# Optimization experiments

Measured on AMD Instinct MI355X. Metric: run time of the kernel, lower is better.

The kernel has to match this reference:

```python
import jax, jax.numpy as jnp
import numpy as np

B_, N, C, H = 512, 49, 256, 8
DH = C // H            # 32
RB, NRF = 8, 32
NWIN = B_ // RB        # 64
DC = 64                # class_token_dim
TC = C + 2 * DC        # 384
WS = 7
SCALE = DH ** -0.5


def _rel_pos_index():
    ch = np.arange(WS)
    coords = np.stack(np.meshgrid(ch, ch, indexing='ij')).reshape(2, -1)  # [2,49]
    rel = (coords[:, :, None] - coords[:, None, :]).transpose(1, 2, 0)    # [49,49,2]
    rel[..., 0] += WS - 1
    rel[..., 1] += WS - 1
    rel[..., 0] *= 2 * WS - 1
    return jnp.asarray(rel.sum(-1).reshape(-1))  # [49*49]


def _ln(x, axes, eps=1e-5):
    m = x.mean(axes, keepdims=True)
    v = x.var(axes, keepdims=True)
    return (x - m) * jax.lax.rsqrt(v + eps)


def setup_inputs() -> dict:
    key = jax.random.key(0)
    ks = jax.random.split(key, 20)
    def w(i, shape, s=0.02):
        return jax.random.normal(ks[i], shape, jnp.float32) * s
    return dict(
        x=w(0, (B_, N, C), 1.0),
        x_ref=w(1, (RB, NRF, C), 1.0),
        depth_token=w(2, (B_, N, DC), 1.0),
        seg_token=w(3, (B_, N, DC), 1.0),
        qkv_w=w(4, (C, 3 * C)), qkv_b=jnp.zeros(3 * C, jnp.float32),
        proj_w=w(5, (C, C)), proj_b=jnp.zeros(C, jnp.float32),
        rel_bias=w(6, ((2 * WS - 1) ** 2, H)),
        diff_mu=w(7, (1, 1, C), 1.0), diff_logsigma=w(8, (1, 1, C)),
        ref_qk_w=w(9, (C, 2 * C)), ref_qk_b=jnp.zeros(2 * C, jnp.float32),
        conv_w=w(10, (H, H, 3, 3), 0.1), conv_b=jnp.zeros(H, jnp.float32),
        q_norm_w=jnp.ones(C, jnp.float32), q_norm_b=jnp.zeros(C, jnp.float32),
        q_proj_w=w(11, (C, C)), q_proj_b=jnp.zeros(C, jnp.float32),
        cls_dth_q_w=w(12, (DC, DC)), cls_dth_q_b=jnp.zeros(DC, jnp.float32),
        cls_seg_q_w=w(13, (DC, DC)), cls_seg_q_b=jnp.zeros(DC, jnp.float32),
        global_k_w=w(14, (TC, TC)), global_k_b=jnp.zeros(TC, jnp.float32),
        global_v_w=w(15, (TC, TC)), global_v_b=jnp.zeros(TC, jnp.float32),
        proj_dth_w=w(16, (DC, DC)), proj_dth_b=jnp.zeros(DC, jnp.float32),
    )


def reference(x, x_ref, depth_token, seg_token, qkv_w, qkv_b, proj_w, proj_b,
              rel_bias, diff_mu, diff_logsigma, ref_qk_w, ref_qk_b, conv_w, conv_b,
              q_norm_w, q_norm_b, q_proj_w, q_proj_b, cls_dth_q_w, cls_dth_q_b,
              cls_seg_q_w, cls_seg_q_b, global_k_w, global_k_b, global_v_w,
              global_v_b, proj_dth_w, proj_dth_b):
    # qkv: [B_,N,3C] -> q,k,v each [B_,H,N,DH]
    qkv = (x @ qkv_w + qkv_b).reshape(B_, N, 3, H, DH).transpose(2, 0, 3, 1, 4)
    q, k, v = qkv[0], qkv[1], qkv[2]

    # ---- group attention (ref branch) ----
    ref_qk = (x_ref @ ref_qk_w + ref_qk_b).reshape(RB, NRF, 2, C).transpose(2, 0, 1, 3)
    ref_q, ref_v = ref_qk[0], ref_qk[1]                       # [RB,NRF,C]
    ref_q = diff_mu + jnp.exp(diff_logsigma) * ref_q
    ref_q = ref_q.reshape(RB, NRF, H, DH).transpose(0, 2, 1, 3)  # [RB,H,NRF,DH]
    ref_v = ref_v.reshape(RB, NRF, H, DH).transpose(0, 2, 1, 3)

    qs = (q * SCALE).reshape(RB, NWIN, H, N, DH)
    # scores against shared (per-image) ref keys; avoids materializing repeated K
    ref_attn = jnp.einsum('rwhnd,rhfd->rhwnf', qs, ref_q)     # [RB,H,NWIN,N,NRF]
    ref_attn_r = ref_attn.reshape(RB, H, NWIN * N, NRF)
    # 3-step diffusion: conv2d over heads-as-channels + LN(no affine) + gelu, residual
    for _ in range(3):
        u = jax.lax.conv_general_dilated(
            ref_attn_r, conv_w, (1, 1), 'SAME',
            dimension_numbers=('NCHW', 'OIHW', 'NCHW')) + conv_b[None, :, None, None]
        u = jax.nn.gelu(_ln(u, (-2, -1)), approximate=False)
        ref_attn_r = ref_attn_r + u
    ref_attn = jax.nn.softmax(ref_attn_r.reshape(RB, H, NWIN, N, NRF), axis=-1)
    q_new = jnp.einsum('rhwnf,rhfd->rwnhd', ref_attn, ref_v).reshape(B_, N, C)
    q_sc = q.transpose(0, 2, 1, 3).reshape(B_, N, C)          # unscaled shortcut
    q_new = (_ln(q_new + q_sc, (-1,)) * q_norm_w + q_norm_b) @ q_proj_w + q_proj_b + q_sc
    q_new = q_new.reshape(B_, N, H, DH).transpose(0, 2, 1, 3) * SCALE

    # ---- window attention with relative position bias ----
    bias = rel_bias[_rel_pos_index()].reshape(N, N, H).transpose(2, 0, 1)  # [H,N,N]
    attn = jax.nn.softmax(jnp.einsum('bhnd,bhmd->bhnm', q_new, k) + bias[None], axis=-1)
    out = jnp.einsum('bhnm,bhmd->bnhd', attn, v).reshape(B_, N, C)
    out = out @ proj_w + proj_b

    # ---- class-token global attention ----
    dch = DC // H   # 8
    tdh = TC // H   # 48
    depth_q = (depth_token @ cls_dth_q_w + cls_dth_q_b).reshape(B_, N, H, dch).transpose(0, 2, 1, 3) * SCALE
    seg_q = (seg_token @ cls_seg_q_w + cls_seg_q_b).reshape(B_, N, H, dch).transpose(0, 2, 1, 3) * SCALE
    t_x = jnp.concatenate([out, depth_token, seg_token], axis=-1)  # [B_,N,TC]
    t_k = (t_x @ global_k_w + global_k_b).reshape(B_, N, H, tdh).transpose(0, 2, 1, 3)
    t_v = (t_x @ global_v_w + global_v_b).reshape(B_, N, H, tdh).transpose(0, 2, 1, 3)

    d_attn = jax.nn.softmax(jnp.einsum('bhnc,bhnt->bhct', depth_q, t_k), axis=-1)
    d_tok = jnp.einsum('bhct,bhnt->bhcn', d_attn, t_v).reshape(B_, DC, N).transpose(0, 2, 1)
    d_tok = d_tok @ proj_dth_w + proj_dth_b
    s_attn = jax.nn.softmax(jnp.einsum('bhnc,bhnt->bhct', seg_q, t_k), axis=-1)
    s_tok = jnp.einsum('bhct,bhnt->bhcn', s_attn, t_v).reshape(B_, DC, N).transpose(0, 2, 1)
    s_tok = s_tok @ proj_dth_w + proj_dth_b  # NOTE: original uses proj_dth for seg too
    return out, d_tok, s_tok
```

## Files before the change

### kernel.cpp

```cpp
#include <hip/hip_runtime.h>
#include <hip/hip_bf16.h>

typedef __hip_bfloat16 bf16;
typedef short s16x8 __attribute__((ext_vector_type(8)));
typedef float f32x4 __attribute__((ext_vector_type(4)));
union V16 { uint4 u4; s16x8 s8; unsigned u[4]; unsigned short s[8]; };

static __device__ __forceinline__ float b2f(bf16 v){ return __bfloat162float(v); }
static __device__ __forceinline__ bf16  f2b(float v){ return __float2bfloat16(v); }
static __device__ __forceinline__ unsigned short f2bs(float x){
    union { float f; unsigned u; } c; c.f = x;
    unsigned r = c.u + 0x7fff + ((c.u >> 16) & 1);
    return (unsigned short)(r >> 16);
}
static __device__ __forceinline__ float bu2f(unsigned short b){
    union { unsigned u; float f; } c; c.u = ((unsigned)b) << 16; return c.f;
}
static __device__ __forceinline__ s16x8 ld16g(const bf16* p){
    V16 u; u.u4 = *(const uint4*)p; return u.s8;
}
static __device__ __forceinline__ void glds16(const void* g, void* l){
    __builtin_amdgcn_global_load_lds(
        (const __attribute__((address_space(1))) unsigned*)g,
        (__attribute__((address_space(3))) unsigned*)l, 16, 0, 0);
}

#define SCALE_T 0.17677669529663687f

__global__ __launch_bounds__(256) void prep_weights(
    const float* __restrict__ qkvw, const float* __restrict__ qpw,
    const float* __restrict__ pw,   const float* __restrict__ gkw,
    const float* __restrict__ gvw,  bf16* __restrict__ Wt)
{
    int idx = blockIdx.x * 256 + threadIdx.x;
    float v;
    if (idx < 196608)      { int j = idx;          int n = j >> 8, k = j & 255; v = qkvw[k * 768 + n]; }
    else if (idx < 262144) { int j = idx - 196608; int n = j >> 8, k = j & 255; v = qpw[k * 256 + n]; }
    else if (idx < 327680) { int j = idx - 262144; int n = j >> 8, k = j & 255; v = pw[k * 256 + n]; }
    else if (idx < 475136) { int j = idx - 327680; int n = j / 384, k = j - n * 384; v = gkw[k * 384 + n]; }
    else                   { int j = idx - 475136; int n = j / 384, k = j - n * 384; v = gvw[k * 384 + n]; }
    ((unsigned short*)Wt)[idx] = f2bs(v);
}

__global__ __launch_bounds__(256) void convert_f32_bf16(
    const float* __restrict__ in, bf16* __restrict__ out)
{
    int i = blockIdx.x * 256 + threadIdx.x;
    float4 v = ((const float4*)in)[i];
    ushort4 o;
    o.x = f2bs(v.x); o.y = f2bs(v.y); o.z = f2bs(v.z); o.w = f2bs(v.w);
    ((ushort4*)out)[i] = o;
}

__global__ __launch_bounds__(256) void tok2b_kernel(
    const float* __restrict__ dth, const float* __restrict__ seg,
    bf16* __restrict__ tokb)
{
    int i = blockIdx.x * 256 + threadIdx.x;
    int row = i >> 4, j8 = i & 15;
    const float* src = (j8 < 8) ? (dth + (size_t)row * 64 + j8 * 8)
                                : (seg + (size_t)row * 64 + (j8 - 8) * 8);
    float4 u0 = ((const float4*)src)[0];
    float4 u1 = ((const float4*)src)[1];
    V16 o;
    o.s[0] = f2bs(u0.x); o.s[1] = f2bs(u0.y);
    o.s[2] = f2bs(u0.z); o.s[3] = f2bs(u0.w);
    o.s[4] = f2bs(u1.x); o.s[5] = f2bs(u1.y);
    o.s[6] = f2bs(u1.z); o.s[7] = f2bs(u1.w);
    *(uint4*)(tokb + (size_t)row * 128 + j8 * 8) = o.u4;
}

template<int TOK>
__global__ __launch_bounds__(256, 2) void gemm_pipe(
    const bf16* __restrict__ A, int lda, const bf16* __restrict__ A2,
    const bf16* __restrict__ Wt, const float* __restrict__ bias,
    const float* __restrict__ bias2,
    const bf16* __restrict__ addp, int addStride,
    float* __restrict__ outF, bf16* __restrict__ outB, int outStrideB,
    int K, int N, float scale)
{
    __shared__ char lds[4][16384];

    const int tid = threadIdx.x;
    const int wv = tid >> 6, lane = tid & 63;
    const int quad = lane >> 4, l15 = lane & 15;
    const int wr = wv >> 1, wc = wv & 1;

    const int gx = (int)gridDim.x;
    const int nwg = gx * (int)gridDim.y;
    int bid = (int)blockIdx.y * gx + (int)blockIdx.x;
    if ((nwg & 7) == 0) bid = (bid & 7) * (nwg >> 3) + (bid >> 3);
    const int bx = bid % gx, by = bid / gx;
    const int rowBase = by * 128, colBase = bx * 128;

    const int srow = tid >> 2;
    const int kOffE = (((tid & 3) ^ ((srow >> 1) & 3)) << 3);

    const unsigned swz = (unsigned)((quad ^ ((l15 >> 1) & 3)) << 4);
    const unsigned aoff0 = (unsigned)(wr * 4096 + l15 * 64) + swz;
    const unsigned boff0 = (unsigned)(wc * 4096 + l15 * 64) + swz;

    f32x4 acc[4][4];
    #pragma unroll
    for (int m = 0; m < 4; ++m)
        #pragma unroll
        for (int n = 0; n < 4; ++n)
            #pragma unroll
            for (int r = 0; r < 4; ++r) acc[m][n][r] = 0.f;

    const int nsteps = K >> 5;

    auto stageN = [&](int i) {
        int kt = i << 5;
        char* base = &lds[i & 3][0];
        #pragma unroll
        for (int c = 0; c < 2; ++c)
            glds16(Wt + (size_t)(colBase + c * 64 + srow) * K + (kt + kOffE),
                   base + 8192 + c * 4096 + tid * 16);
        if (!TOK || kt < 256) {
            #pragma unroll
            for (int c = 0; c < 2; ++c)
                glds16(A + (size_t)(rowBase + c * 64 + srow) * lda + (kt + kOffE),
                       base + c * 4096 + tid * 16);
        } else {
            #pragma unroll
            for (int c = 0; c < 2; ++c)
                glds16(A2 + (size_t)(rowBase + c * 64 + srow) * 128 + (kt - 256 + kOffE),
                       base + c * 4096 + tid * 16);
        }
    };

    stageN(0);
    if (nsteps > 1) stageN(1);
    if (nsteps > 2) stageN(2);

    for (int i = 0; i < nsteps; ++i) {
        int a = nsteps - 1 - i; if (a > 2) a = 2;
        if (a == 2)      asm volatile("s_waitcnt vmcnt(8)" ::: "memory");
        else if (a == 1) asm volatile("s_waitcnt vmcnt(4)" ::: "memory");
        else             asm volatile("s_waitcnt vmcnt(0)" ::: "memory");
        __builtin_amdgcn_sched_barrier(0);
        __builtin_amdgcn_s_barrier();
        __builtin_amdgcn_sched_barrier(0);

        if (i + 3 < nsteps) stageN(i + 3);

        const char* Ab2 = &lds[i & 3][0];
        const char* Bb2 = Ab2 + 8192;
        s16x8 af[4], bfr[4];
        #pragma unroll
        for (int m = 0; m < 4; ++m) af[m]  = *(const s16x8*)(Ab2 + aoff0 + m * 1024);
        #pragma unroll
        for (int n = 0; n < 4; ++n) bfr[n] = *(const s16x8*)(Bb2 + boff0 + n * 1024);
        #pragma unroll
        for (int m = 0; m < 4; ++m)
            #pragma unroll
            for (int n = 0; n < 4; ++n)
                acc[m][n] = __builtin_amdgcn_mfma_f32_16x16x32_bf16(af[m], bfr[n], acc[m][n], 0, 0, 0);
    }

    if (outB) {
        #pragma unroll
        for (int n = 0; n < 4; ++n) {
            int col = colBase + wc * 64 + n * 16 + l15;
            float bb = bias2 ? (col < 384 ? bias[col] : bias2[col - 384]) : bias[col];
            #pragma unroll
            for (int m = 0; m < 4; ++m) {
                #pragma unroll
                for (int r = 0; r < 4; ++r) {
                    int rl = wr * 64 + m * 16 + quad * 4 + r;
                    float v = acc[m][n][r] + bb;
                    if (addp) v += b2f(addp[(size_t)(rowBase + rl) * addStride + col]);
                    v *= scale;
                    if (outF) outF[(size_t)(rowBase + rl) * N + col] = v;
                    int cbyte = (wc * 64 + n * 16 + l15) * 2;
                    int blk = ((cbyte >> 5) ^ ((rl >> 2) & 7)) & 7;
                    *(unsigned short*)((char*)lds + rl * 256 + (blk << 5) + (cbyte & 31)) = f2bs(v);
                }
            }
        }
        __syncthreads();
        #pragma unroll
        for (int i = 0; i < 8; ++i) {
            int lin = i * 256 + tid;
            int rl = lin >> 4, cb = lin & 15;
            int cb2 = ((((cb >> 1) ^ ((rl >> 2) & 7)) & 7) << 1) | (cb & 1);
            uint4 val = *(const uint4*)((const char*)lds + rl * 256 + cb2 * 16);
            *(uint4*)(outB + (size_t)(rowBase + rl) * outStrideB + colBase + cb * 8) = val;
        }
    } else {
        #pragma unroll
        for (int n = 0; n < 4; ++n) {
            int col = colBase + wc * 64 + n * 16 + l15;
            float bb = bias2 ? (col < 384 ? bias[col] : bias2[col - 384]) : bias[col];
            #pragma unroll
            for (int m = 0; m < 4; ++m) {
                #pragma unroll
                for (int r = 0; r < 4; ++r) {
                    int rl = wr * 64 + m * 16 + quad * 4 + r;
                    float v = acc[m][n][r] + bb;
                    if (addp) v += b2f(addp[(size_t)(rowBase + rl) * addStride + col]);
                    v *= scale;
                    if (outF) outF[(size_t)(rowBase + rl) * N + col] = v;
                }
            }
        }
    }
}

template<int AF32, int OF32>
__global__ __launch_bounds__(256) void small64(
    const void* __restrict__ a0, const void* __restrict__ a1,
    const float* __restrict__ w0, const float* __restrict__ w1,
    const float* __restrict__ b0, const float* __restrict__ b1,
    void* __restrict__ o0, void* __restrict__ o1, float scale)
{
    __shared__ unsigned short WT[64 * 72];
    __shared__ float bsh[64];
    const int task = blockIdx.y;
    const void*  A    = task ? a1 : a0;
    const float* W    = task ? w1 : w0;
    const float* bias = task ? b1 : b0;
    void*        outp = task ? o1 : o0;

    int tid = threadIdx.x;
    for (int l = tid; l < 4096; l += 256) {
        int k = l >> 6, n = l & 63;
        WT[n * 72 + k] = f2bs(W[l]);
    }
    if (tid < 64) bsh[tid] = bias[tid];
    __syncthreads();

    const int wv = tid >> 6, lane = tid & 63;
    const int quad = lane >> 4, l15 = lane & 15;
    const int rowBase = blockIdx.x * 64;
    const int arow = rowBase + wv * 16 + l15;

    s16x8 a[2];
    if (AF32) {
        const float* Ar = (const float*)A + (size_t)arow * 64;
        #pragma unroll
        for (int ks = 0; ks < 2; ++ks) {
            float4 u0 = *(const float4*)(Ar + ks * 32 + quad * 8);
            float4 u1 = *(const float4*)(Ar + ks * 32 + quad * 8 + 4);
            V16 o;
            o.s[0] = f2bs(u0.x); o.s[1] = f2bs(u0.y);
            o.s[2] = f2bs(u0.z); o.s[3] = f2bs(u0.w);
            o.s[4] = f2bs(u1.x); o.s[5] = f2bs(u1.y);
            o.s[6] = f2bs(u1.z); o.s[7] = f2bs(u1.w);
            a[ks] = o.s8;
        }
    } else {
        const bf16* Ar = (const bf16*)A + (size_t)arow * 64;
        #pragma unroll
        for (int ks = 0; ks < 2; ++ks)
            a[ks] = ld16g(Ar + ks * 32 + quad * 8);
    }

    f32x4 acc[4];
    #pragma unroll
    for (int n = 0; n < 4; ++n)
        #pragma unroll
        for (int r = 0; r < 4; ++r) acc[n][r] = 0.f;

    #pragma unroll
    for (int ks = 0; ks < 2; ++ks)
        #pragma unroll
        for (int n = 0; n < 4; ++n) {
            s16x8 b = *(const s16x8*)&WT[(n * 16 + l15) * 72 + ks * 32 + quad * 8];
            acc[n] = __builtin_amdgcn_mfma_f32_16x16x32_bf16(a[ks], b, acc[n], 0, 0, 0);
        }

    #pragma unroll
    for (int n = 0; n < 4; ++n) {
        int col = n * 16 + l15;
        float bb = bsh[col];
        #pragma unroll
        for (int r = 0; r < 4; ++r) {
            int row = rowBase + wv * 16 + quad * 4 + r;
            float v = (acc[n][r] + bb) * scale;
            if (OF32) ((float*)outp)[(size_t)row * 64 + col] = v;
            else      ((bf16*)outp)[(size_t)row * 64 + col] = f2b(v);
        }
    }
}

__global__ __launch_bounds__(256) void mfma_gemm(
    const void* __restrict__ A, int a_mode,
    const float* __restrict__ W, const float* __restrict__ bias,
    float* __restrict__ outF, bf16* __restrict__ outB,
    int M, int K, int N, float scale)
{
    __shared__ __hip_bfloat16 Al[64][48];
    __shared__ __hip_bfloat16 Bl[64][48];

    const int tid  = threadIdx.x;
    const int wv   = tid >> 6, lane = tid & 63;
    const int quad = lane >> 4, l15 = lane & 15;
    const int rowBase = blockIdx.y * 64, colBase = blockIdx.x * 64;

    const int am = tid >> 2, ak = (tid & 3) * 8;
    const int bn = tid & 63, bk = (tid >> 6) * 8;

    f32x4 acc[4];
    #pragma unroll
    for (int t = 0; t < 4; ++t)
        #pragma unroll
        for (int r = 0; r < 4; ++r) acc[t][r] = 0.f;

    for (int kt = 0; kt < K; kt += 32) {
        s16x8 sa;
        if (a_mode == 1) {
            const bf16* Ab = (const bf16*)A;
            V16 u; u.u4 = *(const uint4*)(Ab + (size_t)(rowBase + am) * K + kt + ak);
            sa = u.s8;
        } else {
            const float* src = (const float*)A;
            const float4* p = (const float4*)(src + (size_t)(rowBase + am) * K + kt + ak);
            float4 u0 = p[0], u1 = p[1];
            sa[0] = (short)f2bs(u0.x); sa[1] = (short)f2bs(u0.y);
            sa[2] = (short)f2bs(u0.z); sa[3] = (short)f2bs(u0.w);
            sa[4] = (short)f2bs(u1.x); sa[5] = (short)f2bs(u1.y);
            sa[6] = (short)f2bs(u1.z); sa[7] = (short)f2bs(u1.w);
        }
        *(s16x8*)&Al[am][ak] = sa;

        s16x8 sb;
        #pragma unroll
        for (int j = 0; j < 8; ++j)
            sb[j] = (short)f2bs(W[(size_t)(kt + bk + j) * N + colBase + bn]);
        *(s16x8*)&Bl[bn][bk] = sb;

        __syncthreads();

        s16x8 a = *(const s16x8*)&Al[wv * 16 + l15][quad * 8];
        #pragma unroll
        for (int t = 0; t < 4; ++t) {
            s16x8 b = *(const s16x8*)&Bl[t * 16 + l15][quad * 8];
            acc[t] = __builtin_amdgcn_mfma_f32_16x16x32_bf16(a, b, acc[t], 0, 0, 0);
        }
        __syncthreads();
    }

    #pragma unroll
    for (int t = 0; t < 4; ++t) {
        int col = colBase + t * 16 + l15;
        float bb = bias[col];
        #pragma unroll
        for (int r = 0; r < 4; ++r) {
            int row = rowBase + wv * 16 + quad * 4 + r;
            float v = (acc[t][r] + bb) * scale;
            if (outF) outF[(size_t)row * N + col] = v;
            if (outB) outB[(size_t)row * N + col] = f2b(v);
        }
    }
}

__global__ __launch_bounds__(256) void refprep_kernel(
    const float* __restrict__ ref_qk, const float* __restrict__ mu,
    const float* __restrict__ ls, float* __restrict__ ref_q_t,
    float* __restrict__ ref_v_t)
{
    int idx = blockIdx.x * 256 + threadIdx.x;
    int d = idx & 31, f = (idx >> 5) & 31, h = (idx >> 10) & 7, r = idx >> 13;
    int c = h * 32 + d;
    size_t src = (size_t)(r * 32 + f) * 512 + c;
    ref_q_t[idx] = mu[c] + __expf(ls[c]) * ref_qk[src];
    ref_v_t[idx] = ref_qk[src + 256];
}

__global__ __launch_bounds__(256) void refattn_kernel(
    const bf16* __restrict__ qkv, const float* __restrict__ ref_q_t,
    bf16* __restrict__ ref_attn)
{
    int blk = blockIdx.x;
    int w = blk & 63, h = (blk >> 6) & 7, r = blk >> 9;
    int b = r * 64 + w;
    __shared__ float qt[49 * 32];
    __shared__ float rq[32 * 33];
    int tid = threadIdx.x;
    for (int l = tid; l < 1568; l += 256) {
        int n = l >> 5, d = l & 31;
        qt[l] = b2f(qkv[(size_t)(b * 49 + n) * 768 + h * 32 + d]) * SCALE_T;
    }
    for (int l = tid; l < 1024; l += 256) {
        int f = l >> 5, d = l & 31;
        rq[f * 33 + d] = ref_q_t[(size_t)((r * 8 + h) * 32 + f) * 32 + d];
    }
    __syncthreads();
    for (int l = tid; l < 1568; l += 256) {
        int n = l >> 5, f = l & 31;
        float acc = 0.f;
        #pragma unroll
        for (int d2 = 0; d2 < 32; ++d2) acc += qt[n * 32 + d2] * rq[f * 33 + d2];
        ref_attn[(size_t)(((r * 8 + h) * 64 + w) * 49 + n) * 32 + f] = f2b(acc);
    }
}

__global__ __launch_bounds__(256) void conv_kernel(
    const bf16* __restrict__ in, const float* __restrict__ conv_w,
    const float* __restrict__ conv_b, bf16* __restrict__ u)
{
    __shared__ float w_s[576];
    __shared__ float b_s[8];
    int tid = threadIdx.x;
    for (int l = tid; l < 576; l += 256) w_s[l] = conv_w[l];
    if (tid < 8) b_s[tid] = conv_b[tid];
    __syncthreads();

    int idx = blockIdx.x * 256 + tid;
    int fb = idx & 3;
    int p  = (idx >> 2) % 3136;
    int r  = idx / 12544;
    int f0 = fb * 8;

    float acc[8][8];
    #pragma unroll
    for (int o = 0; o < 8; ++o) {
        float bo = b_s[o];
        #pragma unroll
        for (int f = 0; f < 8; ++f) acc[o][f] = bo;
    }

    for (int i = 0; i < 8; ++i) {
        float ext[3][10];
        #pragma unroll
        for (int dy = 0; dy < 3; ++dy) {
            int pp = p + dy - 1;
            bool pv = (unsigned)pp < 3136u;
            size_t base = ((size_t)((r * 8 + i) * 3136 + (pv ? pp : 0))) * 32 + f0;
            V16 uv;
            uv.u4 = pv ? *(const uint4*)(in + base) : make_uint4(0, 0, 0, 0);
            #pragma unroll
            for (int j = 0; j < 8; ++j) {
                unsigned sh = uv.u[j >> 1];
                unsigned bits = (j & 1) ? (sh & 0xffff0000u) : (sh << 16);
                union { unsigned uu; float fl; } cv; cv.uu = bits;
                ext[dy][j + 1] = cv.fl;
            }
            ext[dy][0] = (pv && f0 > 0)      ? b2f(in[base - 1]) : 0.f;
            ext[dy][9] = (pv && f0 + 8 < 32) ? b2f(in[base + 8]) : 0.f;
        }
        #pragma unroll
        for (int o = 0; o < 8; ++o) {
            #pragma unroll
            for (int ky = 0; ky < 3; ++ky) {
                const float* wp = &w_s[((o * 8 + i) * 3 + ky) * 3];
                float w0 = wp[0], w1 = wp[1], w2 = wp[2];
                #pragma unroll
                for (int f = 0; f < 8; ++f)
                    acc[o][f] += ext[ky][f] * w0 + ext[ky][f + 1] * w1 + ext[ky][f + 2] * w2;
            }
        }
    }

    #pragma unroll
    for (int o = 0; o < 8; ++o) {
        bf16 ov[8];
        #pragma unroll
        for (int f = 0; f < 8; ++f) ov[f] = f2b(acc[o][f]);
        *(uint4*)(u + ((size_t)((r * 8 + o) * 3136 + p)) * 32 + f0) = *(uint4*)ov;
    }
}

__global__ __launch_bounds__(256) void lnstats_kernel(
    const bf16* __restrict__ u, float* __restrict__ stats4)
{
    int g4 = blockIdx.x;
    const bf16* p = u + (size_t)g4 * 25088;
    int tid = threadIdx.x;
    float s = 0.f, s2 = 0.f;
    for (int it = tid; it < 3136; it += 256) {
        V16 uv; uv.u4 = *(const uint4*)(p + it * 8);
        #pragma unroll
        for (int j = 0; j < 8; ++j) {
            unsigned sh = uv.u[j >> 1];
            unsigned bits = (j & 1) ? (sh & 0xffff0000u) : (sh << 16);
            union { unsigned uu; float fl; } cv; cv.uu = bits;
            s += cv.fl; s2 += cv.fl * cv.fl;
        }
    }
    __shared__ float r1[256], r2[256];
    r1[tid] = s; r2[tid] = s2; __syncthreads();
    for (int st = 128; st > 0; st >>= 1) {
        if (tid < st) { r1[tid] += r1[tid + st]; r2[tid] += r2[tid + st]; }
        __syncthreads();
    }
    if (tid == 0) {
        stats4[g4 * 2]     = r1[0];
        stats4[g4 * 2 + 1] = r2[0];
    }
}

__global__ __launch_bounds__(256) void lngelu_kernel(
    const bf16* __restrict__ u, const float* __restrict__ stats4,
    bf16* __restrict__ ref_attn)
{
    int idx8 = blockIdx.x * 256 + threadIdx.x;
    int g = idx8 / 12544;
    size_t base = (size_t)idx8 * 8;
    float sum = 0.f, sq = 0.f;
    #pragma unroll
    for (int q = 0; q < 4; ++q) {
        sum += stats4[(g * 4 + q) * 2];
        sq  += stats4[(g * 4 + q) * 2 + 1];
    }
    float mean = sum * (1.f / 100352.f);
    float var  = sq * (1.f / 100352.f) - mean * mean;
    var = fmaxf(var, 0.f);
    float rstd = rsqrtf(var + 1e-5f);
    V16 uv; uv.u4 = *(const uint4*)(u + base);
    V16 rv; rv.u4 = *(const uint4*)(ref_attn + base);
    bf16 outv[8];
    #pragma unroll
    for (int j = 0; j < 8; ++j) {
        unsigned shu = uv.u[j >> 1];
        unsigned shr = rv.u[j >> 1];
        unsigned bu = (j & 1) ? (shu & 0xffff0000u) : (shu << 16);
        unsigned br = (j & 1) ? (shr & 0xffff0000u) : (shr << 16);
        union { unsigned uu; float fl; } cu, cr; cu.uu = bu; cr.uu = br;
        float v = (cu.fl - mean) * rstd;
        float ge = 0.5f * v * (1.f + erff(v * 0.7071067811865476f));
        outv[j] = f2b(cr.fl + ge);
    }
    *(uint4*)(ref_attn + base) = *(uint4*)outv;
}

__global__ __launch_bounds__(256) void qnew_pre_kernel(
    const bf16* __restrict__ qkv, const bf16* __restrict__ ref_attn,
    const float* __restrict__ ref_v_t,
    const float* __restrict__ qnw, const float* __restrict__ qnb,
    bf16* __restrict__ ln_t)
{
    int ww = threadIdx.x >> 6, lane = threadIdx.x & 63;
    int row = blockIdx.x * 4 + ww;
    int b = row / 49, n = row % 49;
    int r = b >> 6, w = b & 63;
    int h = lane >> 3, d0 = (lane & 7) * 4;

    const bf16* la = ref_attn + ((size_t)(((r * 8 + h) * 64 + w) * 49 + n)) * 32 + d0;
    ushort4 lu = *(const ushort4*)la;
    float lg[4] = { bu2f(lu.x), bu2f(lu.y), bu2f(lu.z), bu2f(lu.w) };

    float m = fmaxf(fmaxf(lg[0], lg[1]), fmaxf(lg[2], lg[3]));
    m = fmaxf(m, __shfl_xor(m, 1));
    m = fmaxf(m, __shfl_xor(m, 2));
    m = fmaxf(m, __shfl_xor(m, 4));
    float p[4], s = 0.f;
    #pragma unroll
    for (int j = 0; j < 4; ++j) { p[j] = __expf(lg[j] - m); s += p[j]; }
    s += __shfl_xor(s, 1);
    s += __shfl_xor(s, 2);
    s += __shfl_xor(s, 4);
    float inv = 1.f / s;
    #pragma unroll
    for (int j = 0; j < 4; ++j) p[j] *= inv;

    const float* rv = ref_v_t + ((size_t)(r * 8 + h) * 32) * 32 + d0;
    float y[4] = {0.f, 0.f, 0.f, 0.f};
    #pragma unroll
    for (int f = 0; f < 32; ++f) {
        int src = (lane & 56) | (f >> 2);
        float pf = __shfl(p[f & 3], src);
        float4 rvf = *(const float4*)(rv + f * 32);
        y[0] += pf * rvf.x; y[1] += pf * rvf.y;
        y[2] += pf * rvf.z; y[3] += pf * rvf.w;
    }

    ushort4 qu = *(const ushort4*)(qkv + (size_t)row * 768 + lane * 4);
    float z[4] = { y[0] + bu2f(qu.x), y[1] + bu2f(qu.y),
                   y[2] + bu2f(qu.z), y[3] + bu2f(qu.w) };

    float s1 = z[0] + z[1] + z[2] + z[3];
    #pragma unroll
    for (int off = 1; off < 64; off <<= 1) s1 += __shfl_xor(s1, off);
    float mean = s1 * (1.f / 256.f);
    float zc[4] = { z[0] - mean, z[1] - mean, z[2] - mean, z[3] - mean };
    float s2 = zc[0]*zc[0] + zc[1]*zc[1] + zc[2]*zc[2] + zc[3]*zc[3];
    #pragma unroll
    for (int off = 1; off < 64; off <<= 1) s2 += __shfl_xor(s2, off);
    float rstd = rsqrtf(s2 * (1.f / 256.f) + 1e-5f);

    float4 wv = *(const float4*)(qnw + lane * 4);
    float4 bv = *(const float4*)(qnb + lane * 4);
    bf16 outv[4];
    outv[0] = f2b(zc[0] * rstd * wv.x + bv.x);
    outv[1] = f2b(zc[1] * rstd * wv.y + bv.y);
    outv[2] = f2b(zc[2] * rstd * wv.z + bv.z);
    outv[3] = f2b(zc[3] * rstd * wv.w + bv.w);
    *(ushort4*)(ln_t + (size_t)row * 256 + lane * 4) = *(ushort4*)outv;
}

__global__ __launch_bounds__(256) void winattn_kernel(
    const bf16* __restrict__ qkv, const bf16* __restrict__ q_new,
    const float* __restrict__ rel_bias, bf16* __restrict__ attn_out)
{
    const int wv = threadIdx.x >> 6, lane = threadIdx.x & 63;
    const int quad = lane >> 4, l15 = lane & 15;
    const int b = blockIdx.x >> 1;
    const int h = (blockIdx.x & 1) * 4 + wv;

    __shared__ bf16 lds[4 * 6912];
    bf16* P  = &lds[wv * 6912];
    bf16* vT = P + 4608;

    {
        int m = lane;
        if (m < 49) {
            const bf16* vp = qkv + ((size_t)(b * 49 + m)) * 768 + 512 + h * 32;
            V16 v0, v1, v2, v3;
            v0.u4 = *(const uint4*)(vp);
            v1.u4 = *(const uint4*)(vp + 8);
            v2.u4 = *(const uint4*)(vp + 16);
            v3.u4 = *(const uint4*)(vp + 24);
            #pragma unroll
            for (int d = 0; d < 8; ++d) {
                ((unsigned short*)vT)[d * 72 + m]        = v0.s[d];
                ((unsigned short*)vT)[(d + 8) * 72 + m]  = v1.s[d];
                ((unsigned short*)vT)[(d + 16) * 72 + m] = v2.s[d];
                ((unsigned short*)vT)[(d + 24) * 72 + m] = v3.s[d];
            }
        } else {
            #pragma unroll
            for (int d = 0; d < 32; ++d)
                ((unsigned short*)vT)[d * 72 + m] = 0;
        }
    }

    s16x8 aq[4], bk[4];
    #pragma unroll
    for (int t = 0; t < 4; ++t) {
        int qr = t * 16 + l15; qr = qr > 48 ? 48 : qr;
        aq[t] = ld16g(q_new + ((size_t)(b * 49 + qr)) * 256 + h * 32 + quad * 8);
        bk[t] = ld16g(qkv + ((size_t)(b * 49 + qr)) * 768 + 256 + h * 32 + quad * 8);
    }
    f32x4 S[4][4];
    #pragma unroll
    for (int tn = 0; tn < 4; ++tn)
        #pragma unroll
        for (int tm = 0; tm < 4; ++tm) {
            #pragma unroll
            for (int r = 0; r < 4; ++r) S[tn][tm][r] = 0.f;
            S[tn][tm] = __builtin_amdgcn_mfma_f32_16x16x32_bf16(aq[tn], bk[tm], S[tn][tm], 0, 0, 0);
        }

    int mvalid[4], mi[4], mj[4];
    #pragma unroll
    for (int tm = 0; tm < 4; ++tm) {
        int m0 = tm * 16 + l15;
        mvalid[tm] = (m0 < 49);
        int mc = m0 > 48 ? 48 : m0;
        mi[tm] = mc / 7; mj[tm] = mc - mi[tm] * 7;
    }
    #pragma unroll
    for (int tn = 0; tn < 4; ++tn) {
        #pragma unroll
        for (int r = 0; r < 4; ++r) {
            int n0 = tn * 16 + quad * 4 + r;
            int nc = n0 > 48 ? 48 : n0;
            int ni = nc / 7, nj = nc - (nc / 7) * 7;
            float vals[4];
            float mx = -1e30f;
            #pragma unroll
            for (int tm = 0; tm < 4; ++tm) {
                float v = S[tn][tm][r]
                        + rel_bias[((ni - mi[tm] + 6) * 13 + (nj - mj[tm] + 6)) * 8 + h];
                if (!mvalid[tm]) v = -1e30f;
                vals[tm] = v;
                mx = fmaxf(mx, v);
            }
            mx = fmaxf(mx, __shfl_xor(mx, 1));
            mx = fmaxf(mx, __shfl_xor(mx, 2));
            mx = fmaxf(mx, __shfl_xor(mx, 4));
            mx = fmaxf(mx, __shfl_xor(mx, 8));
            float s = 0.f;
            #pragma unroll
            for (int tm = 0; tm < 4; ++tm) { vals[tm] = __expf(vals[tm] - mx); s += vals[tm]; }
            s += __shfl_xor(s, 1);
            s += __shfl_xor(s, 2);
            s += __shfl_xor(s, 4);
            s += __shfl_xor(s, 8);
            float inv = 1.f / s;
            #pragma unroll
            for (int tm = 0; tm < 4; ++tm)
                ((unsigned short*)P)[n0 * 72 + tm * 16 + l15] = f2bs(vals[tm] * inv);
        }
    }

    f32x4 O[4][2];
    #pragma unroll
    for (int tn = 0; tn < 4; ++tn)
        #pragma unroll
        for (int td = 0; td < 2; ++td)
            #pragma unroll
            for (int r = 0; r < 4; ++r) O[tn][td][r] = 0.f;

    #pragma unroll
    for (int ks = 0; ks < 2; ++ks) {
        s16x8 bv0 = *(const s16x8*)&vT[(0 * 16 + l15) * 72 + ks * 32 + quad * 8];
        s16x8 bv1 = *(const s16x8*)&vT[(1 * 16 + l15) * 72 + ks * 32 + quad * 8];
        #pragma unroll
        for (int tn = 0; tn < 4; ++tn) {
            s16x8 ap = *(const s16x8*)&P[(tn * 16 + l15) * 72 + ks * 32 + quad * 8];
            O[tn][0] = __builtin_amdgcn_mfma_f32_16x16x32_bf16(ap, bv0, O[tn][0], 0, 0, 0);
            O[tn][1] = __builtin_amdgcn_mfma_f32_16x16x32_bf16(ap, bv1, O[tn][1], 0, 0, 0);
        }
    }

    #pragma unroll
    for (int tn = 0; tn < 4; ++tn)
        #pragma unroll
        for (int r = 0; r < 4; ++r) {
            int n0 = tn * 16 + quad * 4 + r;
            if (n0 < 49) {
                size_t base = ((size_t)(b * 49 + n0)) * 256 + h * 32;
                attn_out[base + l15]      = f2b(O[tn][0][r]);
                attn_out[base + 16 + l15] = f2b(O[tn][1][r]);
            }
        }
}

__global__ __launch_bounds__(256) void clsattn_kernel(
    const bf16* __restrict__ tkv,
    const bf16* __restrict__ depth_q, const bf16* __restrict__ seg_q,
    bf16* __restrict__ d_pre, bf16* __restrict__ s_pre)
{
    const int wv = threadIdx.x >> 6, lane = threadIdx.x & 63;
    const int quad = lane >> 4, l15 = lane & 15;
    const int bh = blockIdx.x * 4 + wv;
    const int b = bh >> 3, h = bh & 7;

    __shared__ bf16 lds[4 * 5760];
    unsigned short* QP = (unsigned short*)&lds[wv * 5760];
    unsigned short* KV = QP + 1152;

    {
        int n = lane;
        V16 dv, sv;
        if (n < 49) {
            dv.u4 = *(const uint4*)(depth_q + ((size_t)(b * 49 + n)) * 64 + h * 8);
            sv.u4 = *(const uint4*)(seg_q   + ((size_t)(b * 49 + n)) * 64 + h * 8);
        } else {
            dv.u4 = make_uint4(0, 0, 0, 0); sv.u4 = make_uint4(0, 0, 0, 0);
        }
        #pragma unroll
        for (int c = 0; c < 8; ++c) {
            QP[c * 72 + n]       = dv.s[c];
            QP[(8 + c) * 72 + n] = sv.s[c];
        }
    }
    {
        int n = lane;
        V16 k[6];
        if (n < 49) {
            const bf16* kp = tkv + ((size_t)(b * 49 + n)) * 768 + h * 48;
            #pragma unroll
            for (int c6 = 0; c6 < 6; ++c6) k[c6].u4 = *(const uint4*)(kp + c6 * 8);
        } else {
            #pragma unroll
            for (int c6 = 0; c6 < 6; ++c6) k[c6].u4 = make_uint4(0, 0, 0, 0);
        }
        #pragma unroll
        for (int c6 = 0; c6 < 6; ++c6)
            #pragma unroll
            for (int j = 0; j < 8; ++j)
                KV[(c6 * 8 + j) * 72 + n] = k[c6].s[j];
    }

    f32x4 S[3];
    #pragma unroll
    for (int t3 = 0; t3 < 3; ++t3)
        #pragma unroll
        for (int r = 0; r < 4; ++r) S[t3][r] = 0.f;
    #pragma unroll
    for (int ks = 0; ks < 2; ++ks) {
        s16x8 a = *(const s16x8*)&QP[l15 * 72 + ks * 32 + quad * 8];
        #pragma unroll
        for (int t3 = 0; t3 < 3; ++t3) {
            s16x8 bf = *(const s16x8*)&KV[(t3 * 16 + l15) * 72 + ks * 32 + quad * 8];
            S[t3] = __builtin_amdgcn_mfma_f32_16x16x32_bf16(a, bf, S[t3], 0, 0, 0);
        }
    }

    #pragma unroll
    for (int r = 0; r < 4; ++r) {
        float v0 = S[0][r], v1 = S[1][r], v2 = S[2][r];
        float mx = fmaxf(fmaxf(v0, v1), v2);
        mx = fmaxf(mx, __shfl_xor(mx, 1));
        mx = fmaxf(mx, __shfl_xor(mx, 2));
        mx = fmaxf(mx, __shfl_xor(mx, 4));
        mx = fmaxf(mx, __shfl_xor(mx, 8));
        float e0 = __expf(v0 - mx), e1 = __expf(v1 - mx), e2 = __expf(v2 - mx);
        float s = e0 + e1 + e2;
        s += __shfl_xor(s, 1);
        s += __shfl_xor(s, 2);
        s += __shfl_xor(s, 4);
        s += __shfl_xor(s, 8);
        float inv = 1.f / s;
        int c = quad * 4 + r;
        QP[c * 72 + 0 * 16 + l15] = f2bs(e0 * inv);
        QP[c * 72 + 1 * 16 + l15] = f2bs(e1 * inv);
        QP[c * 72 + 2 * 16 + l15] = f2bs(e2 * inv);
    }
    #pragma unroll
    for (int z = 0; z < 4; ++z)
        QP[(lane & 15) * 72 + 48 + (lane >> 4) * 4 + z] = 0;

    {
        int n = lane;
        V16 v[6], zv; zv.u4 = make_uint4(0, 0, 0, 0);
        if (n < 49) {
            const bf16* vp = tkv + ((size_t)(b * 49 + n)) * 768 + 384 + h * 48;
            #pragma unroll
            for (int c6 = 0; c6 < 6; ++c6) v[c6].u4 = *(const uint4*)(vp + c6 * 8);
        } else {
            #pragma unroll
            for (int c6 = 0; c6 < 6; ++c6) v[c6].u4 = zv.u4;
        }
        #pragma unroll
        for (int c6 = 0; c6 < 6; ++c6)
            *(uint4*)&KV[n * 72 + c6 * 8] = v[c6].u4;
        *(uint4*)&KV[n * 72 + 48] = zv.u4;
        *(uint4*)&KV[n * 72 + 56] = zv.u4;
    }

    f32x4 O[4];
    #pragma unroll
    for (int t4 = 0; t4 < 4; ++t4)
        #pragma unroll
        for (int r = 0; r < 4; ++r) O[t4][r] = 0.f;
    #pragma unroll
    for (int ks = 0; ks < 2; ++ks) {
        s16x8 a = *(const s16x8*)&QP[l15 * 72 + ks * 32 + quad * 8];
        #pragma unroll
        for (int t4 = 0; t4 < 4; ++t4) {
            s16x8 bf = *(const s16x8*)&KV[(t4 * 16 + l15) * 72 + ks * 32 + quad * 8];
            O[t4] = __builtin_amdgcn_mfma_f32_16x16x32_bf16(a, bf, O[t4], 0, 0, 0);
        }
    }

    #pragma unroll
    for (int t4 = 0; t4 < 4; ++t4) {
        int n = t4 * 16 + l15;
        if (n < 49) {
            size_t base = ((size_t)(b * 49 + n)) * 64 + h * 8;
            #pragma unroll
            for (int r = 0; r < 4; ++r) {
                int c = quad * 4 + r;
                if (c < 8) d_pre[base + c] = f2b(O[t4][r]);
                else       s_pre[base + c - 8] = f2b(O[t4][r]);
            }
        }
    }
}

extern "C" void kernel_launch(void* const* d_in, const int* in_sizes, int n_in,
                              void* d_out, int out_size, void* d_ws, size_t ws_size,
                              hipStream_t stream)
{
    const float* x          = (const float*)d_in[0];
    const float* x_ref      = (const float*)d_in[1];
    const float* dth_tok    = (const float*)d_in[2];
    const float* seg_tok    = (const float*)d_in[3];
    const float* qkv_w      = (const float*)d_in[4];
    const float* qkv_b      = (const float*)d_in[5];
    const float* proj_w     = (const float*)d_in[6];
    const float* proj_b     = (const float*)d_in[7];
    const float* rel_bias   = (const float*)d_in[8];
    const float* diff_mu    = (const float*)d_in[9];
    const float* diff_ls    = (const float*)d_in[10];
    const float* ref_qk_w   = (const float*)d_in[11];
    const float* ref_qk_b   = (const float*)d_in[12];
    const float* conv_w     = (const float*)d_in[13];
    const float* conv_b     = (const float*)d_in[14];
    const float* q_norm_w   = (const float*)d_in[15];
    const float* q_norm_b   = (const float*)d_in[16];
    const float* q_proj_w   = (const float*)d_in[17];
    const float* q_proj_b   = (const float*)d_in[18];
    const float* cls_dth_w  = (const float*)d_in[19];
    const float* cls_dth_b  = (const float*)d_in[20];
    const float* cls_seg_w  = (const float*)d_in[21];
    const float* cls_seg_b  = (const float*)d_in[22];
    const float* glob_k_w   = (const float*)d_in[23];
    const float* glob_k_b   = (const float*)d_in[24];
    const float* glob_v_w   = (const float*)d_in[25];
    const float* glob_v_b   = (const float*)d_in[26];
    const float* proj_dth_w = (const float*)d_in[27];
    const float* proj_dth_b = (const float*)d_in[28];

    bf16* wsb = (bf16*)d_ws;
    bf16* qkv      = wsb;
    bf16* tkv      = wsb;
    bf16* ref_attn = wsb + 19267584;
    bf16* q_new    = ref_attn;
    bf16* out0b    = ref_attn;
    bf16* depth_q  = ref_attn;
    bf16* seg_q    = ref_attn + 1605632;
    bf16* d_pre    = ref_attn + 3211264;
    bf16* s_pre    = ref_attn + 4816896;
    bf16* u_buf    = wsb + 25690112;
    bf16* xb       = u_buf;
    bf16* ln_t     = u_buf;
    bf16* attn_out = u_buf;
    float* ref_qk  = (float*)((char*)d_ws + 64225280);
    float* ref_q_t = ref_qk + 131072;
    float* ref_v_t = ref_q_t + 65536;
    float* stats4  = ref_qk;

    float* out0  = (float*)d_out;
    float* out_d = out0 + 6422528;
    float* out_s = out0 + 8028160;

    bf16* Wt_all = (bf16*)out_d;
    bf16* tokb   = (bf16*)out_s;

    prep_weights<<<2432, 256, 0, stream>>>(qkv_w, q_proj_w, proj_w, glob_k_w, glob_v_w, Wt_all);
    convert_f32_bf16<<<6272, 256, 0, stream>>>(x, xb);
    tok2b_kernel<<<1568, 256, 0, stream>>>(dth_tok, seg_tok, tokb);

    gemm_pipe<0><<<dim3(6, 196), 256, 0, stream>>>(xb, 256, nullptr,
        Wt_all, qkv_b, nullptr, nullptr, 0, nullptr, qkv, 768, 256, 768, 1.f);
    mfma_gemm<<<dim3(8, 4), 256, 0, stream>>>(x_ref, 0, ref_qk_w, ref_qk_b,
                                              ref_qk, nullptr, 256, 256, 512, 1.f);
    refprep_kernel<<<256, 256, 0, stream>>>(ref_qk, diff_mu, diff_ls, ref_q_t, ref_v_t);
    refattn_kernel<<<4096, 256, 0, stream>>>(qkv, ref_q_t, ref_attn);
    for (int it = 0; it < 3; ++it) {
        conv_kernel<<<392, 256, 0, stream>>>(ref_attn, conv_w, conv_b, u_buf);
        lnstats_kernel<<<256, 256, 0, stream>>>(u_buf, stats4);
        lngelu_kernel<<<3136, 256, 0, stream>>>(u_buf, stats4, ref_attn);
    }
    qnew_pre_kernel<<<6272, 256, 0, stream>>>(qkv, ref_attn, ref_v_t,
                                              q_norm_w, q_norm_b, ln_t);
    gemm_pipe<0><<<dim3(2, 196), 256, 0, stream>>>(ln_t, 256, nullptr,
        Wt_all + 196608, q_proj_b, nullptr, qkv, 768, nullptr, q_new, 256, 256, 256, SCALE_T);
    winattn_kernel<<<1024, 256, 0, stream>>>(qkv, q_new, rel_bias, attn_out);
    gemm_pipe<0><<<dim3(2, 196), 256, 0, stream>>>(attn_out, 256, nullptr,
        Wt_all + 262144, proj_b, nullptr, nullptr, 0, out0, out0b, 256, 256, 256, 1.f);
    gemm_pipe<1><<<dim3(6, 196), 256, 0, stream>>>(out0b, 256, tokb,
        Wt_all + 327680, glob_k_b, glob_v_b, nullptr, 0, nullptr, tkv, 768, 384, 768, 1.f);
    small64<1, 0><<<dim3(392, 2), 256, 0, stream>>>(dth_tok, seg_tok,
        cls_dth_w, cls_seg_w, cls_dth_b, cls_seg_b, depth_q, seg_q, SCALE_T);
    clsattn_kernel<<<1024, 256, 0, stream>>>(tkv, depth_q, seg_q, d_pre, s_pre);
    small64<0, 1><<<dim3(392, 2), 256, 0, stream>>>(d_pre, s_pre,
        proj_dth_w, proj_dth_w, proj_dth_b, proj_dth_b, out_d, out_s, 1.f);
}
```

Baseline: 496.3 us.

## Use MFMA for reference attention and merge input conversion kernels

The reference-attention score kernel changes from a scalar LDS dot-product loop to bf16 MFMA 16x16x32 instructions. Each wave handles one window and head, loading Q fragments directly from the qkv buffer and a pre-scaled bf16 reference query written by refprep. The three prep/convert kernels are also merged into a single launch to cut launch overhead. Casting the reference query to bf16 and folding the scale in before the cast can change rounding slightly.

```diff
diff --git a/kernel.cpp b/kernel.cpp
--- a/kernel.cpp
+++ b/kernel.cpp
@@ -27,47 +27,44 @@
 
 #define SCALE_T 0.17677669529663687f
 
-__global__ __launch_bounds__(256) void prep_weights(
+__global__ __launch_bounds__(256) void prep_all(
     const float* __restrict__ qkvw, const float* __restrict__ qpw,
     const float* __restrict__ pw,   const float* __restrict__ gkw,
-    const float* __restrict__ gvw,  bf16* __restrict__ Wt)
-{
-    int idx = blockIdx.x * 256 + threadIdx.x;
-    float v;
-    if (idx < 196608)      { int j = idx;          int n = j >> 8, k = j & 255; v = qkvw[k * 768 + n]; }
-    else if (idx < 262144) { int j = idx - 196608; int n = j >> 8, k = j & 255; v = qpw[k * 256 + n]; }
-    else if (idx < 327680) { int j = idx - 262144; int n = j >> 8, k = j & 255; v = pw[k * 256 + n]; }
-    else if (idx < 475136) { int j = idx - 327680; int n = j / 384, k = j - n * 384; v = gkw[k * 384 + n]; }
-    else                   { int j = idx - 475136; int n = j / 384, k = j - n * 384; v = gvw[k * 384 + n]; }
-    ((unsigned short*)Wt)[idx] = f2bs(v);
-}
-
-__global__ __launch_bounds__(256) void convert_f32_bf16(
-    const float* __restrict__ in, bf16* __restrict__ out)
-{
-    int i = blockIdx.x * 256 + threadIdx.x;
-    float4 v = ((const float4*)in)[i];
-    ushort4 o;
-    o.x = f2bs(v.x); o.y = f2bs(v.y); o.z = f2bs(v.z); o.w = f2bs(v.w);
-    ((ushort4*)out)[i] = o;
-}
-
-__global__ __launch_bounds__(256) void tok2b_kernel(
-    const float* __restrict__ dth, const float* __restrict__ seg,
+    const float* __restrict__ gvw,  bf16* __restrict__ Wt,
+    const float* __restrict__ x,    bf16* __restrict__ xb,
+    const float* __restrict__ dth,  const float* __restrict__ seg,
     bf16* __restrict__ tokb)
 {
-    int i = blockIdx.x * 256 + threadIdx.x;
-    int row = i >> 4, j8 = i & 15;
-    const float* src = (j8 < 8) ? (dth + (size_t)row * 64 + j8 * 8)
-                                : (seg + (size_t)row * 64 + (j8 - 8) * 8);
-    float4 u0 = ((const float4*)src)[0];
-    float4 u1 = ((const float4*)src)[1];
-    V16 o;
-    o.s[0] = f2bs(u0.x); o.s[1] = f2bs(u0.y);
-    o.s[2] = f2bs(u0.z); o.s[3] = f2bs(u0.w);
-    o.s[4] = f2bs(u1.x); o.s[5] = f2bs(u1.y);
-    o.s[6] = f2bs(u1.z); o.s[7] = f2bs(u1.w);
-    *(uint4*)(tokb + (size_t)row * 128 + j8 * 8) = o.u4;
+    int blk = blockIdx.x, tid = threadIdx.x;
+    if (blk < 2432) {
+        int idx = blk * 256 + tid;
+        float v;
+        if (idx < 196608)      { int j = idx;          int n = j >> 8, k = j & 255; v = qkvw[k * 768 + n]; }
+        else if (idx < 262144) { int j = idx - 196608; int n = j >> 8, k = j & 255; v = qpw[k * 256 + n]; }
+        else if (idx < 327680) { int j = idx - 262144; int n = j >> 8, k = j & 255; v = pw[k * 256 + n]; }
+        else if (idx < 475136) { int j = idx - 327680; int n = j / 384, k = j - n * 384; v = gkw[k * 384 + n]; }
+        else                   { int j = idx - 475136; int n = j / 384, k = j - n * 384; v = gvw[k * 384 + n]; }
+        ((unsigned short*)Wt)[idx] = f2bs(v);
+    } else if (blk < 8704) {
+        int i = (blk - 2432) * 256 + tid;
+        float4 v = ((const float4*)x)[i];
+        ushort4 o;
+        o.x = f2bs(v.x); o.y = f2bs(v.y); o.z = f2bs(v.z); o.w = f2bs(v.w);
+        ((ushort4*)xb)[i] = o;
+    } else {
+        int i = (blk - 8704) * 256 + tid;
+        int row = i >> 4, j8 = i & 15;
+        const float* src = (j8 < 8) ? (dth + (size_t)row * 64 + j8 * 8)
+                                    : (seg + (size_t)row * 64 + (j8 - 8) * 8);
+        float4 u0 = ((const float4*)src)[0];
+        float4 u1 = ((const float4*)src)[1];
+        V16 o;
+        o.s[0] = f2bs(u0.x); o.s[1] = f2bs(u0.y);
+        o.s[2] = f2bs(u0.z); o.s[3] = f2bs(u0.w);
+        o.s[4] = f2bs(u1.x); o.s[5] = f2bs(u1.y);
+        o.s[6] = f2bs(u1.z); o.s[7] = f2bs(u1.w);
+        *(uint4*)(tokb + (size_t)row * 128 + j8 * 8) = o.u4;
+    }
 }
 
 template<int TOK>
@@ -358,42 +355,56 @@
 
 __global__ __launch_bounds__(256) void refprep_kernel(
     const float* __restrict__ ref_qk, const float* __restrict__ mu,
-    const float* __restrict__ ls, float* __restrict__ ref_q_t,
+    const float* __restrict__ ls, bf16* __restrict__ rq_b,
     float* __restrict__ ref_v_t)
 {
     int idx = blockIdx.x * 256 + threadIdx.x;
-    int d = idx & 31, f = (idx >> 5) & 31, h = (idx >> 10) & 7, r = idx >> 13;
+    int d = idx & 31, h = (idx >> 10) & 7;
     int c = h * 32 + d;
+    int f = (idx >> 5) & 31, r = idx >> 13;
     size_t src = (size_t)(r * 32 + f) * 512 + c;
-    ref_q_t[idx] = mu[c] + __expf(ls[c]) * ref_qk[src];
+    ((unsigned short*)rq_b)[idx] = f2bs((mu[c] + __expf(ls[c]) * ref_qk[src]) * SCALE_T);
     ref_v_t[idx] = ref_qk[src + 256];
 }
 
 __global__ __launch_bounds__(256) void refattn_kernel(
-    const bf16* __restrict__ qkv, const float* __restrict__ ref_q_t,
+    const bf16* __restrict__ qkv, const bf16* __restrict__ rq_b,
     bf16* __restrict__ ref_attn)
 {
+    const int wv = threadIdx.x >> 6, lane = threadIdx.x & 63;
+    const int quad = lane >> 4, l15 = lane & 15;
     int blk = blockIdx.x;
-    int w = blk & 63, h = (blk >> 6) & 7, r = blk >> 9;
-    int b = r * 64 + w;
-    __shared__ float qt[49 * 32];
-    __shared__ float rq[32 * 33];
-    int tid = threadIdx.x;
-    for (int l = tid; l < 1568; l += 256) {
-        int n = l >> 5, d = l & 31;
-        qt[l] = b2f(qkv[(size_t)(b * 49 + n) * 768 + h * 32 + d]) * SCALE_T;
-    }
-    for (int l = tid; l < 1024; l += 256) {
-        int f = l >> 5, d = l & 31;
-        rq[f * 33 + d] = ref_q_t[(size_t)((r * 8 + h) * 32 + f) * 32 + d];
-    }
-    __syncthreads();
-    for (int l = tid; l < 1568; l += 256) {
-        int n = l >> 5, f = l & 31;
-        float acc = 0.f;
-        #pragma unroll
-        for (int d2 = 0; d2 < 32; ++d2) acc += qt[n * 32 + d2] * rq[f * 33 + d2];
-        ref_attn[(size_t)(((r * 8 + h) * 64 + w) * 49 + n) * 32 + f] = f2b(acc);
+    int rh = blk >> 4;
+    int h = rh & 7;
+    int w = (blk & 15) * 4 + wv;
+    int b = (rh >> 3) * 64 + w;
+
+    s16x8 bk0 = ld16g(rq_b + ((size_t)(rh * 32 + l15)) * 32 + quad * 8);
+    s16x8 bk1 = ld16g(rq_b + ((size_t)(rh * 32 + 16 + l15)) * 32 + quad * 8);
+
+    s16x8 aq[4];
+    #pragma unroll
+    for (int t = 0; t < 4; ++t) {
+        int qr = t * 16 + l15; qr = qr > 48 ? 48 : qr;
+        aq[t] = ld16g(qkv + ((size_t)(b * 49 + qr)) * 768 + h * 32 + quad * 8);
+    }
+
+    #pragma unroll
+    for (int t = 0; t < 4; ++t) {
+        f32x4 S0, S1;
+        #pragma unroll
+        for (int r = 0; r < 4; ++r) { S0[r] = 0.f; S1[r] = 0.f; }
+        S0 = __builtin_amdgcn_mfma_f32_16x16x32_bf16(aq[t], bk0, S0, 0, 0, 0);
+        S1 = __builtin_amdgcn_mfma_f32_16x16x32_bf16(aq[t], bk1, S1, 0, 0, 0);
+        #pragma unroll
+        for (int r = 0; r < 4; ++r) {
+            int n0 = t * 16 + quad * 4 + r;
+            if (n0 < 49) {
+                size_t base = ((size_t)(rh * 64 + w) * 49 + n0) * 32;
+                ref_attn[base + l15]      = f2b(S0[r]);
+                ref_attn[base + 16 + l15] = f2b(S1[r]);
+            }
+        }
     }
 }
 
@@ -903,8 +914,8 @@
     bf16* ln_t     = u_buf;
     bf16* attn_out = u_buf;
     float* ref_qk  = (float*)((char*)d_ws + 64225280);
-    float* ref_q_t = ref_qk + 131072;
-    float* ref_v_t = ref_q_t + 65536;
+    bf16*  rq_b    = (bf16*)(ref_qk + 131072);
+    float* ref_v_t = ref_qk + 131072 + 65536;
     float* stats4  = ref_qk;
 
     float* out0  = (float*)d_out;
@@ -914,16 +925,15 @@
     bf16* Wt_all = (bf16*)out_d;
     bf16* tokb   = (bf16*)out_s;
 
-    prep_weights<<<2432, 256, 0, stream>>>(qkv_w, q_proj_w, proj_w, glob_k_w, glob_v_w, Wt_all);
-    convert_f32_bf16<<<6272, 256, 0, stream>>>(x, xb);
-    tok2b_kernel<<<1568, 256, 0, stream>>>(dth_tok, seg_tok, tokb);
+    prep_all<<<10272, 256, 0, stream>>>(qkv_w, q_proj_w, proj_w, glob_k_w, glob_v_w,
+                                        Wt_all, x, xb, dth_tok, seg_tok, tokb);
 
     gemm_pipe<0><<<dim3(6, 196), 256, 0, stream>>>(xb, 256, nullptr,
         Wt_all, qkv_b, nullptr, nullptr, 0, nullptr, qkv, 768, 256, 768, 1.f);
     mfma_gemm<<<dim3(8, 4), 256, 0, stream>>>(x_ref, 0, ref_qk_w, ref_qk_b,
                                               ref_qk, nullptr, 256, 256, 512, 1.f);
-    refprep_kernel<<<256, 256, 0, stream>>>(ref_qk, diff_mu, diff_ls, ref_q_t, ref_v_t);
-    refattn_kernel<<<4096, 256, 0, stream>>>(qkv, ref_q_t, ref_attn);
+    refprep_kernel<<<256, 256, 0, stream>>>(ref_qk, diff_mu, diff_ls, rq_b, ref_v_t);
+    refattn_kernel<<<1024, 256, 0, stream>>>(qkv, rq_b, ref_attn);
     for (int it = 0; it < 3; ++it) {
         conv_kernel<<<392, 256, 0, stream>>>(ref_attn, conv_w, conv_b, u_buf);
         lnstats_kernel<<<256, 256, 0, stream>>>(u_buf, stats4);
```

Measured after the change: 477.2 us. -3.9%, faster.
